# Kernel tuning notes

Measured on AMD Instinct MI355X. Metric: run time of the kernel, lower is better.

## Reference

```python
import jax, jax.numpy as jnp
import numpy as np

B, L, H, W, C = 2, 5, 48, 176, 256
HEADS, DIM_HEAD = 8, 32
INNER = HEADS * DIM_HEAD  # 256
SCALE = DIM_HEAD ** -0.5


def setup_inputs() -> dict:
    key = jax.random.key(0)
    k1, k2, k3, k4, k5 = jax.random.split(key, 5)
    x = jax.random.normal(k1, (B, L, H, W, C), dtype=jnp.float32)
    # mask of shape (B, H, W, 1, L); slot 0 always valid so no softmax row is fully masked
    mask = jax.random.randint(k2, (B, H, W, 1, L), 0, 2, dtype=jnp.int32)
    mask = mask.at[..., 0].set(1)
    w_qkv = jax.random.normal(k3, (C, 3 * INNER), dtype=jnp.float32) / np.sqrt(C)
    w_out = jax.random.normal(k4, (INNER, C), dtype=jnp.float32) / np.sqrt(INNER)
    b_out = jax.random.normal(k5, (C,), dtype=jnp.float32) * 0.01
    return {"x": x, "mask": mask, "w_qkv": w_qkv, "w_out": w_out, "b_out": b_out}


def reference(x, mask, w_qkv, w_out, b_out):
    # x: (B, L, H, W, C) -> (B, H, W, L, C)
    xp = jnp.transpose(x, (0, 2, 3, 1, 4))
    qkv = xp @ w_qkv  # (B, H, W, L, 3*INNER)
    q, k, v = jnp.split(qkv, 3, axis=-1)
    # split heads: (B, H, W, L, M, D)
    shp = (B, H, W, L, HEADS, DIM_HEAD)
    q = q.reshape(shp)
    k = k.reshape(shp)
    v = v.reshape(shp)
    # attention over the small CAV axis L
    att = jnp.einsum('bhwimd,bhwjmd->bmhwij', q, k) * SCALE  # (B,M,H,W,L,L)
    m = mask[:, None]  # (B,1,H,W,1,L) broadcasts over (B,M,H,W,i,j)
    att = jnp.where(m == 0, -jnp.inf, att)
    att = jax.nn.softmax(att, axis=-1)
    out = jnp.einsum('bmhwij,bhwjmd->bhwimd', att, v)  # (B,H,W,L,M,D)
    out = out.reshape(B, H, W, L, INNER)
    out = out @ w_out + b_out  # dropout is identity in eval
    return jnp.transpose(out, (0, 3, 1, 2, 4))  # (B, L, H, W, C)
```

## Files before the change

### kernel.cpp

```cpp
#include <hip/hip_runtime.h>


typedef __attribute__((ext_vector_type(8))) short short8;
typedef __attribute__((ext_vector_type(4))) float f32x4;

#define SCALE_F 0.17677669529663687f

static __device__ __forceinline__ float b2f(unsigned short u) {
    union { unsigned u; float f; } x; x.u = ((unsigned)u) << 16; return x.f;
}
static __device__ __forceinline__ unsigned short f2b(float f) {
    union { float f; unsigned u; } x; x.f = f;
    unsigned u = x.u;
    return (unsigned short)((u + 0x7FFFu + ((u >> 16) & 1u)) >> 16);
}

static __device__ __forceinline__ size_t row_to_xoff(int r) {
    int l = r % 5; int t = r / 5;
    int w = t % 176; t /= 176;
    int h = t % 48; int b = t / 48;
    return (size_t)(((b * 5 + l) * 48 + h) * 176 + w) * 256;
}

static __device__ __forceinline__ int lidx(int r, int c) {
    return r * 256 + ((((c >> 3) ^ (r & 7)) << 3) | (c & 7));
}

static __device__ __forceinline__ void async_cp16(const unsigned short* g, unsigned short* l) {
    __builtin_amdgcn_global_load_lds(
        (__attribute__((address_space(1))) void*)(void*)g,
        (__attribute__((address_space(3))) void*)(void*)l, 16, 0, 0);
}

static __device__ __forceinline__ void barrier_lgkm() {
    __builtin_amdgcn_s_waitcnt(0xC07F);
    __builtin_amdgcn_s_barrier();
}

__global__ __launch_bounds__(256) void k_prep(const float* __restrict__ wq,
                                              const float* __restrict__ wo,
                                              unsigned short* __restrict__ wqt,
                                              unsigned short* __restrict__ wot) {
    int i = blockIdx.x * 256 + threadIdx.x;
    if (i < 196608) { int k = i / 768, n = i % 768; wqt[n * 256 + k] = f2b(wq[i]); }
    if (i < 65536)  { int k = i / 256, n = i % 256; wot[n * 256 + k] = f2b(wo[i]); }
}

template<int C>
static __device__ __forceinline__ void issue_chunk(const unsigned short* __restrict__ wqt,
                                                   const unsigned short* __restrict__ wot,
                                                   unsigned short* __restrict__ Bw,
                                                   int n0w, int lane) {
    constexpr int p = C >> 3;
    constexpr int kk = C & 7;
    constexpr int slot = C & 1;
    const unsigned short* wbase = (p < 3) ? (wqt + p * 65536) : wot;
#pragma unroll
    for (int t = 0; t < 4; ++t) {
        int cidx = t * 64 + lane;
        int nl = cidx >> 2;
        int kq = (cidx & 3) ^ ((nl >> 1) & 3);
        const unsigned short* g = wbase + (n0w + nl) * 256 + kk * 32 + kq * 8;
        async_cp16(g, Bw + slot * 2048 + t * 512);
    }
}

template<int C>
static __device__ __forceinline__ void chunk_step(f32x4 (&acc)[5][4],
        const unsigned short* __restrict__ As, unsigned short* __restrict__ Bw,
        const unsigned short* __restrict__ wqt, const unsigned short* __restrict__ wot,
        int n0w, int lane) {
    constexpr int kk = C & 7;
    constexpr int slot = C & 1;
    constexpr int imm = (C == 31) ? 0xF70 : 0xF74;
    const int ln = lane & 15, quad = lane >> 4;
    __builtin_amdgcn_s_waitcnt(imm);
    short8 b[4];
#pragma unroll
    for (int n = 0; n < 4; ++n)
        b[n] = *(const short8*)&Bw[slot * 2048 + (n * 16 + ln) * 32
                                   + ((quad ^ ((ln >> 1) & 3)) * 8)];
    __builtin_amdgcn_s_waitcnt(0xC07F);
    if constexpr (C + 2 < 32) issue_chunk<C + 2>(wqt, wot, Bw, n0w, lane);
    short8 a[5];
#pragma unroll
    for (int m = 0; m < 5; ++m)
        a[m] = *(const short8*)&As[lidx(m * 16 + ln, kk * 32 + quad * 8)];
#pragma unroll
    for (int m = 0; m < 5; ++m)
#pragma unroll
        for (int n = 0; n < 4; ++n)
            acc[m][n] = __builtin_amdgcn_mfma_f32_16x16x32_bf16(a[m], b[n], acc[m][n], 0, 0, 0);
}

template<int P>
static __device__ __forceinline__ void gemm8(f32x4 (&acc)[5][4],
        const unsigned short* __restrict__ As, unsigned short* __restrict__ Bw,
        const unsigned short* __restrict__ wqt, const unsigned short* __restrict__ wot,
        int n0w, int lane) {
    chunk_step<P * 8 + 0>(acc, As, Bw, wqt, wot, n0w, lane);
    chunk_step<P * 8 + 1>(acc, As, Bw, wqt, wot, n0w, lane);
    chunk_step<P * 8 + 2>(acc, As, Bw, wqt, wot, n0w, lane);
    chunk_step<P * 8 + 3>(acc, As, Bw, wqt, wot, n0w, lane);
    chunk_step<P * 8 + 4>(acc, As, Bw, wqt, wot, n0w, lane);
    chunk_step<P * 8 + 5>(acc, As, Bw, wqt, wot, n0w, lane);
    chunk_step<P * 8 + 6>(acc, As, Bw, wqt, wot, n0w, lane);
    chunk_step<P * 8 + 7>(acc, As, Bw, wqt, wot, n0w, lane);
}

static __device__ __forceinline__ void cstore(const f32x4 (&acc)[5][4],
        unsigned short* __restrict__ Ds, int n0w, int lane) {
    const int ln = lane & 15, quad = lane >> 4;
#pragma unroll
    for (int m = 0; m < 5; ++m)
#pragma unroll
        for (int n = 0; n < 4; ++n)
#pragma unroll
            for (int rg = 0; rg < 4; ++rg)
                Ds[lidx(m * 16 + quad * 4 + rg, n0w + n * 16 + ln)] = f2b(acc[m][n][rg]);
}

__global__ __launch_bounds__(256, 1) void k_fused(const float* __restrict__ x,
                                                  const int* __restrict__ mask,
                                                  const unsigned short* __restrict__ wqt,
                                                  const unsigned short* __restrict__ wot,
                                                  const float* __restrict__ bo,
                                                  float* __restrict__ out) {
    __shared__ __align__(16) unsigned short xs[80 * 256];
    __shared__ __align__(16) unsigned short qs[80 * 256];
    __shared__ __align__(16) unsigned short kvs[80 * 256];
    __shared__ __align__(16) unsigned short Bb[4 * 4096];

    const int tid = threadIdx.x;
    const int blk = blockIdx.x;
    const int rbase = blk * 80;
    const int lane = tid & 63, wv = tid >> 6;
    const int n0w = wv * 64;
    unsigned short* Bw = Bb + wv * 4096;

#pragma unroll
    for (int i = 0; i < 10; ++i) {
        int u = i * 256 + tid;
        int r = u >> 5, cb = u & 31;
        size_t xo = row_to_xoff(rbase + r) + cb * 8;
        float4 v0 = *(const float4*)(x + xo);
        float4 v1 = *(const float4*)(x + xo + 4);
        short8 o;
        o[0] = (short)f2b(v0.x); o[1] = (short)f2b(v0.y);
        o[2] = (short)f2b(v0.z); o[3] = (short)f2b(v0.w);
        o[4] = (short)f2b(v1.x); o[5] = (short)f2b(v1.y);
        o[6] = (short)f2b(v1.z); o[7] = (short)f2b(v1.w);
        *(short8*)&xs[lidx(r, cb * 8)] = o;
    }

    const int part = tid & 3, hh = (tid >> 2) & 7, g8 = tid >> 5;
    int mka[5], mkb[5];
#pragma unroll
    for (int j = 0; j < 5; ++j) {
        mka[j] = mask[(blk * 16 + g8) * 5 + j];
        mkb[j] = mask[(blk * 16 + g8 + 8) * 5 + j];
    }

    issue_chunk<0>(wqt, wot, Bw, n0w, lane);
    issue_chunk<1>(wqt, wot, Bw, n0w, lane);

    barrier_lgkm();

    {
        f32x4 acc[5][4];
#pragma unroll
        for (int m = 0; m < 5; ++m)
#pragma unroll
            for (int n = 0; n < 4; ++n) acc[m][n] = (f32x4){0.f, 0.f, 0.f, 0.f};
        gemm8<0>(acc, xs, Bw, wqt, wot, n0w, lane);
        cstore(acc, qs, n0w, lane);
    }
    {
        f32x4 acc[5][4];
#pragma unroll
        for (int m = 0; m < 5; ++m)
#pragma unroll
            for (int n = 0; n < 4; ++n) acc[m][n] = (f32x4){0.f, 0.f, 0.f, 0.f};
        gemm8<1>(acc, xs, Bw, wqt, wot, n0w, lane);
        cstore(acc, kvs, n0w, lane);
    }
    barrier_lgkm();

    float pr[2][5][5];
#pragma unroll
    for (int rep = 0; rep < 2; ++rep) {
        const int g = g8 + rep * 8;
        const int c0 = hh * 32 + part * 8;
        float qf[5][8];
#pragma unroll
        for (int i = 0; i < 5; ++i) {
            short8 qv = *(const short8*)&qs[lidx(g * 5 + i, c0)];
#pragma unroll
            for (int d = 0; d < 8; ++d) qf[i][d] = b2f((unsigned short)qv[d]);
        }
        float s[5][5];
#pragma unroll
        for (int j = 0; j < 5; ++j) {
            short8 kv = *(const short8*)&kvs[lidx(g * 5 + j, c0)];
            float kf[8];
#pragma unroll
            for (int d = 0; d < 8; ++d) kf[d] = b2f((unsigned short)kv[d]);
#pragma unroll
            for (int i = 0; i < 5; ++i) {
                float acc = 0.f;
#pragma unroll
                for (int d = 0; d < 8; ++d) acc += qf[i][d] * kf[d];
                s[i][j] = acc;
            }
        }
#pragma unroll
        for (int i = 0; i < 5; ++i)
#pragma unroll
            for (int j = 0; j < 5; ++j) {
                s[i][j] += __shfl_xor(s[i][j], 1, 64);
                s[i][j] += __shfl_xor(s[i][j], 2, 64);
            }
        int mcur[5];
#pragma unroll
        for (int j = 0; j < 5; ++j) mcur[j] = rep ? mkb[j] : mka[j];
#pragma unroll
        for (int i = 0; i < 5; ++i) {
            float mx = -1e30f;
#pragma unroll
            for (int j = 0; j < 5; ++j) {
                s[i][j] = mcur[j] ? s[i][j] * SCALE_F : -1e30f;
                mx = fmaxf(mx, s[i][j]);
            }
            float sum = 0.f;
#pragma unroll
            for (int j = 0; j < 5; ++j) { pr[rep][i][j] = __expf(s[i][j] - mx); sum += pr[rep][i][j]; }
            float inv = 1.f / sum;
#pragma unroll
            for (int j = 0; j < 5; ++j) pr[rep][i][j] *= inv;
        }
    }
    barrier_lgkm();

    {
        f32x4 acc[5][4];
#pragma unroll
        for (int m = 0; m < 5; ++m)
#pragma unroll
            for (int n = 0; n < 4; ++n) acc[m][n] = (f32x4){0.f, 0.f, 0.f, 0.f};
        gemm8<2>(acc, xs, Bw, wqt, wot, n0w, lane);
        cstore(acc, kvs, n0w, lane);
    }
    barrier_lgkm();

#pragma unroll
    for (int rep = 0; rep < 2; ++rep) {
        const int g = g8 + rep * 8;
        const int c0 = hh * 32 + part * 8;
        float o[5][8];
#pragma unroll
        for (int i = 0; i < 5; ++i)
#pragma unroll
            for (int d = 0; d < 8; ++d) o[i][d] = 0.f;
#pragma unroll
        for (int j = 0; j < 5; ++j) {
            short8 vv = *(const short8*)&kvs[lidx(g * 5 + j, c0)];
            float vf[8];
#pragma unroll
            for (int d = 0; d < 8; ++d) vf[d] = b2f((unsigned short)vv[d]);
#pragma unroll
            for (int i = 0; i < 5; ++i)
#pragma unroll
                for (int d = 0; d < 8; ++d) o[i][d] += pr[rep][i][j] * vf[d];
        }
#pragma unroll
        for (int i = 0; i < 5; ++i) {
            short8 ov;
#pragma unroll
            for (int d = 0; d < 8; ++d) ov[d] = (short)f2b(o[i][d]);
            *(short8*)&kvs[lidx(g * 5 + i, c0)] = ov;
        }
    }
    barrier_lgkm();

    {
        f32x4 acc[5][4];
#pragma unroll
        for (int m = 0; m < 5; ++m)
#pragma unroll
            for (int n = 0; n < 4; ++n) acc[m][n] = (f32x4){0.f, 0.f, 0.f, 0.f};
        gemm8<3>(acc, kvs, Bw, wqt, wot, n0w, lane);
        const int ln = lane & 15, quad = lane >> 4;
        float bv[4];
#pragma unroll
        for (int n = 0; n < 4; ++n) bv[n] = bo[n0w + n * 16 + ln];
#pragma unroll
        for (int m = 0; m < 5; ++m)
#pragma unroll
            for (int rg = 0; rg < 4; ++rg) {
                int row = m * 16 + quad * 4 + rg;
                size_t off = row_to_xoff(rbase + row);
#pragma unroll
                for (int n = 0; n < 4; ++n)
                    out[off + n0w + n * 16 + ln] = acc[m][n][rg] + bv[n];
            }
    }
}

extern "C" void kernel_launch(void* const* d_in, const int* in_sizes, int n_in,
                              void* d_out, int out_size, void* d_ws, size_t ws_size,
                              hipStream_t stream) {
    const float* x   = (const float*)d_in[0];
    const int* mask  = (const int*)d_in[1];
    const float* wq  = (const float*)d_in[2];
    const float* wo  = (const float*)d_in[3];
    const float* bo  = (const float*)d_in[4];
    float* out = (float*)d_out;

    char* ws = (char*)d_ws;
    unsigned short* wqt = (unsigned short*)(ws);
    unsigned short* wot = (unsigned short*)(ws + 393216);

    hipLaunchKernelGGL(k_prep, dim3(768), dim3(256), 0, stream, wq, wo, wqt, wot);
    hipLaunchKernelGGL(k_fused, dim3(1056), dim3(256), 0, stream, x, mask, wqt, wot, bo, out);
}
```

Measured before the change: 263.5 us.

## Double block threads to 512 with each wave covering 32 output columns

Grows the fused block from 4 to 8 waves. Each wave now owns a 32-column slice of every GEMM (5x2 MFMA tiles instead of 5x4), and each thread handles one token group in the attention phase instead of two. The per-wave weight staging buffer shrinks so total shared memory is unchanged, and the async wait counts are adjusted for two copies per chunk. This is meant to give more waves per CU to hide latency. In exchange, each wave does less MFMA work per A-fragment load, so shared-memory reads of the activation tile are duplicated across twice as many waves.

```diff
diff --git a/kernel.cpp b/kernel.cpp
--- a/kernel.cpp
+++ b/kernel.cpp
@@ -56,29 +56,29 @@
     constexpr int slot = C & 1;
     const unsigned short* wbase = (p < 3) ? (wqt + p * 65536) : wot;
 #pragma unroll
-    for (int t = 0; t < 4; ++t) {
+    for (int t = 0; t < 2; ++t) {
         int cidx = t * 64 + lane;
         int nl = cidx >> 2;
         int kq = (cidx & 3) ^ ((nl >> 1) & 3);
         const unsigned short* g = wbase + (n0w + nl) * 256 + kk * 32 + kq * 8;
-        async_cp16(g, Bw + slot * 2048 + t * 512);
+        async_cp16(g, Bw + slot * 1024 + t * 512);
     }
 }
 
 template<int C>
-static __device__ __forceinline__ void chunk_step(f32x4 (&acc)[5][4],
+static __device__ __forceinline__ void chunk_step(f32x4 (&acc)[5][2],
         const unsigned short* __restrict__ As, unsigned short* __restrict__ Bw,
         const unsigned short* __restrict__ wqt, const unsigned short* __restrict__ wot,
         int n0w, int lane) {
     constexpr int kk = C & 7;
     constexpr int slot = C & 1;
-    constexpr int imm = (C == 31) ? 0xF70 : 0xF74;
+    constexpr int imm = (C == 31) ? 0xF70 : 0xF72;
     const int ln = lane & 15, quad = lane >> 4;
     __builtin_amdgcn_s_waitcnt(imm);
-    short8 b[4];
-#pragma unroll
-    for (int n = 0; n < 4; ++n)
-        b[n] = *(const short8*)&Bw[slot * 2048 + (n * 16 + ln) * 32
+    short8 b[2];
+#pragma unroll
+    for (int n = 0; n < 2; ++n)
+        b[n] = *(const short8*)&Bw[slot * 1024 + (n * 16 + ln) * 32
                                    + ((quad ^ ((ln >> 1) & 3)) * 8)];
     __builtin_amdgcn_s_waitcnt(0xC07F);
     if constexpr (C + 2 < 32) issue_chunk<C + 2>(wqt, wot, Bw, n0w, lane);
@@ -89,12 +89,12 @@
 #pragma unroll
     for (int m = 0; m < 5; ++m)
 #pragma unroll
-        for (int n = 0; n < 4; ++n)
+        for (int n = 0; n < 2; ++n)
             acc[m][n] = __builtin_amdgcn_mfma_f32_16x16x32_bf16(a[m], b[n], acc[m][n], 0, 0, 0);
 }
 
 template<int P>
-static __device__ __forceinline__ void gemm8(f32x4 (&acc)[5][4],
+static __device__ __forceinline__ void gemm8(f32x4 (&acc)[5][2],
         const unsigned short* __restrict__ As, unsigned short* __restrict__ Bw,
         const unsigned short* __restrict__ wqt, const unsigned short* __restrict__ wot,
         int n0w, int lane) {
@@ -108,19 +108,19 @@
     chunk_step<P * 8 + 7>(acc, As, Bw, wqt, wot, n0w, lane);
 }
 
-static __device__ __forceinline__ void cstore(const f32x4 (&acc)[5][4],
+static __device__ __forceinline__ void cstore(const f32x4 (&acc)[5][2],
         unsigned short* __restrict__ Ds, int n0w, int lane) {
     const int ln = lane & 15, quad = lane >> 4;
 #pragma unroll
     for (int m = 0; m < 5; ++m)
 #pragma unroll
-        for (int n = 0; n < 4; ++n)
+        for (int n = 0; n < 2; ++n)
 #pragma unroll
             for (int rg = 0; rg < 4; ++rg)
                 Ds[lidx(m * 16 + quad * 4 + rg, n0w + n * 16 + ln)] = f2b(acc[m][n][rg]);
 }
 
-__global__ __launch_bounds__(256, 1) void k_fused(const float* __restrict__ x,
+__global__ __launch_bounds__(512, 2) void k_fused(const float* __restrict__ x,
                                                   const int* __restrict__ mask,
                                                   const unsigned short* __restrict__ wqt,
                                                   const unsigned short* __restrict__ wot,
@@ -129,18 +129,18 @@
     __shared__ __align__(16) unsigned short xs[80 * 256];
     __shared__ __align__(16) unsigned short qs[80 * 256];
     __shared__ __align__(16) unsigned short kvs[80 * 256];
-    __shared__ __align__(16) unsigned short Bb[4 * 4096];
+    __shared__ __align__(16) unsigned short Bb[8 * 2048];
 
     const int tid = threadIdx.x;
     const int blk = blockIdx.x;
     const int rbase = blk * 80;
     const int lane = tid & 63, wv = tid >> 6;
-    const int n0w = wv * 64;
-    unsigned short* Bw = Bb + wv * 4096;
-
-#pragma unroll
-    for (int i = 0; i < 10; ++i) {
-        int u = i * 256 + tid;
+    const int n0w = wv * 32;
+    unsigned short* Bw = Bb + wv * 2048;
+
+#pragma unroll
+    for (int i = 0; i < 5; ++i) {
+        int u = i * 512 + tid;
         int r = u >> 5, cb = u & 31;
         size_t xo = row_to_xoff(rbase + r) + cb * 8;
         float4 v0 = *(const float4*)(x + xo);
@@ -153,13 +153,10 @@
         *(short8*)&xs[lidx(r, cb * 8)] = o;
     }
 
-    const int part = tid & 3, hh = (tid >> 2) & 7, g8 = tid >> 5;
-    int mka[5], mkb[5];
-#pragma unroll
-    for (int j = 0; j < 5; ++j) {
-        mka[j] = mask[(blk * 16 + g8) * 5 + j];
-        mkb[j] = mask[(blk * 16 + g8 + 8) * 5 + j];
-    }
+    const int part = tid & 3, hh = (tid >> 2) & 7, g = tid >> 5;
+    int mk[5];
+#pragma unroll
+    for (int j = 0; j < 5; ++j) mk[j] = mask[(blk * 16 + g) * 5 + j];
 
     issue_chunk<0>(wqt, wot, Bw, n0w, lane);
     issue_chunk<1>(wqt, wot, Bw, n0w, lane);
@@ -167,29 +164,27 @@
     barrier_lgkm();
 
     {
-        f32x4 acc[5][4];
-#pragma unroll
-        for (int m = 0; m < 5; ++m)
-#pragma unroll
-            for (int n = 0; n < 4; ++n) acc[m][n] = (f32x4){0.f, 0.f, 0.f, 0.f};
+        f32x4 acc[5][2];
+#pragma unroll
+        for (int m = 0; m < 5; ++m)
+#pragma unroll
+            for (int n = 0; n < 2; ++n) acc[m][n] = (f32x4){0.f, 0.f, 0.f, 0.f};
         gemm8<0>(acc, xs, Bw, wqt, wot, n0w, lane);
         cstore(acc, qs, n0w, lane);
     }
     {
-        f32x4 acc[5][4];
-#pragma unroll
-        for (int m = 0; m < 5; ++m)
-#pragma unroll
-            for (int n = 0; n < 4; ++n) acc[m][n] = (f32x4){0.f, 0.f, 0.f, 0.f};
+        f32x4 acc[5][2];
+#pragma unroll
+        for (int m = 0; m < 5; ++m)
+#pragma unroll
+            for (int n = 0; n < 2; ++n) acc[m][n] = (f32x4){0.f, 0.f, 0.f, 0.f};
         gemm8<1>(acc, xs, Bw, wqt, wot, n0w, lane);
         cstore(acc, kvs, n0w, lane);
     }
     barrier_lgkm();
 
-    float pr[2][5][5];
-#pragma unroll
-    for (int rep = 0; rep < 2; ++rep) {
-        const int g = g8 + rep * 8;
+    float pr[5][5];
+    {
         const int c0 = hh * 32 + part * 8;
         float qf[5][8];
 #pragma unroll
@@ -220,41 +215,36 @@
                 s[i][j] += __shfl_xor(s[i][j], 1, 64);
                 s[i][j] += __shfl_xor(s[i][j], 2, 64);
             }
-        int mcur[5];
-#pragma unroll
-        for (int j = 0; j < 5; ++j) mcur[j] = rep ? mkb[j] : mka[j];
 #pragma unroll
         for (int i = 0; i < 5; ++i) {
             float mx = -1e30f;
 #pragma unroll
             for (int j = 0; j < 5; ++j) {
-                s[i][j] = mcur[j] ? s[i][j] * SCALE_F : -1e30f;
+                s[i][j] = mk[j] ? s[i][j] * SCALE_F : -1e30f;
                 mx = fmaxf(mx, s[i][j]);
             }
             float sum = 0.f;
 #pragma unroll
-            for (int j = 0; j < 5; ++j) { pr[rep][i][j] = __expf(s[i][j] - mx); sum += pr[rep][i][j]; }
+            for (int j = 0; j < 5; ++j) { pr[i][j] = __expf(s[i][j] - mx); sum += pr[i][j]; }
             float inv = 1.f / sum;
 #pragma unroll
-            for (int j = 0; j < 5; ++j) pr[rep][i][j] *= inv;
-        }
-    }
-    barrier_lgkm();
-
-    {
-        f32x4 acc[5][4];
-#pragma unroll
-        for (int m = 0; m < 5; ++m)
-#pragma unroll
-            for (int n = 0; n < 4; ++n) acc[m][n] = (f32x4){0.f, 0.f, 0.f, 0.f};
+            for (int j = 0; j < 5; ++j) pr[i][j] *= inv;
+        }
+    }
+    barrier_lgkm();
+
+    {
+        f32x4 acc[5][2];
+#pragma unroll
+        for (int m = 0; m < 5; ++m)
+#pragma unroll
+            for (int n = 0; n < 2; ++n) acc[m][n] = (f32x4){0.f, 0.f, 0.f, 0.f};
         gemm8<2>(acc, xs, Bw, wqt, wot, n0w, lane);
         cstore(acc, kvs, n0w, lane);
     }
     barrier_lgkm();
 
-#pragma unroll
-    for (int rep = 0; rep < 2; ++rep) {
-        const int g = g8 + rep * 8;
+    {
         const int c0 = hh * 32 + part * 8;
         float o[5][8];
 #pragma unroll
@@ -270,7 +260,7 @@
 #pragma unroll
             for (int i = 0; i < 5; ++i)
 #pragma unroll
-                for (int d = 0; d < 8; ++d) o[i][d] += pr[rep][i][j] * vf[d];
+                for (int d = 0; d < 8; ++d) o[i][d] += pr[i][j] * vf[d];
         }
 #pragma unroll
         for (int i = 0; i < 5; ++i) {
@@ -283,16 +273,16 @@
     barrier_lgkm();
 
     {
-        f32x4 acc[5][4];
-#pragma unroll
-        for (int m = 0; m < 5; ++m)
-#pragma unroll
-            for (int n = 0; n < 4; ++n) acc[m][n] = (f32x4){0.f, 0.f, 0.f, 0.f};
+        f32x4 acc[5][2];
+#pragma unroll
+        for (int m = 0; m < 5; ++m)
+#pragma unroll
+            for (int n = 0; n < 2; ++n) acc[m][n] = (f32x4){0.f, 0.f, 0.f, 0.f};
         gemm8<3>(acc, kvs, Bw, wqt, wot, n0w, lane);
         const int ln = lane & 15, quad = lane >> 4;
-        float bv[4];
-#pragma unroll
-        for (int n = 0; n < 4; ++n) bv[n] = bo[n0w + n * 16 + ln];
+        float bv[2];
+#pragma unroll
+        for (int n = 0; n < 2; ++n) bv[n] = bo[n0w + n * 16 + ln];
 #pragma unroll
         for (int m = 0; m < 5; ++m)
 #pragma unroll
@@ -300,7 +290,7 @@
                 int row = m * 16 + quad * 4 + rg;
                 size_t off = row_to_xoff(rbase + row);
 #pragma unroll
-                for (int n = 0; n < 4; ++n)
+                for (int n = 0; n < 2; ++n)
                     out[off + n0w + n * 16 + ln] = acc[m][n][rg] + bv[n];
             }
     }
@@ -321,5 +311,5 @@
     unsigned short* wot = (unsigned short*)(ws + 393216);
 
     hipLaunchKernelGGL(k_prep, dim3(768), dim3(256), 0, stream, wq, wo, wqt, wot);
-    hipLaunchKernelGGL(k_fused, dim3(1056), dim3(256), 0, stream, x, mask, wqt, wot, bo, out);
-}
+    hipLaunchKernelGGL(k_fused, dim3(1056), dim3(512), 0, stream, x, mask, wqt, wot, bo, out);
+}
```

Measured after the change: 243.6 us. 7.5% less time.
